# Kernel optimization log

Hardware: AMD Instinct MI355X
Metric: run time of the kernel (lower is better)

Reference implementation:

```python
import jax, jax.numpy as jnp
import numpy as np

N_NODES = 50000
N_EDGES = 800000
HID = 64
N_LAYERS = 3
N_GRAPHS = 64
NEG_SLOPE = 0.01  # nn.LeakyReLU default


def setup_inputs() -> dict:
    key = jax.random.key(0)
    ks = jax.random.split(key, 10)
    return {
        "x": jax.random.normal(ks[0], (N_NODES, HID), dtype=jnp.float32),
        "edge_attr": jax.random.normal(ks[1], (N_EDGES,), dtype=jnp.float32),
        "edge_w": jax.random.normal(ks[2], (N_LAYERS, 1, HID), dtype=jnp.float32) * 0.1,
        "edge_b": jax.random.normal(ks[3], (N_LAYERS, HID), dtype=jnp.float32) * 0.1,
        "node_w": jax.random.normal(ks[4], (N_LAYERS, 2 * HID, HID), dtype=jnp.float32) * 0.05,
        "node_b": jax.random.normal(ks[5], (N_LAYERS, HID), dtype=jnp.float32) * 0.1,
        "fc_w": jax.random.normal(ks[6], (HID, 1), dtype=jnp.float32) * 0.1,
        "fc_b": jax.random.normal(ks[7], (1,), dtype=jnp.float32) * 0.1,
        "edge_index": jax.random.randint(ks[8], (2, N_EDGES), 0, N_NODES, dtype=jnp.int32),
        "batch": jnp.sort(jax.random.randint(ks[9], (N_NODES,), 0, N_GRAPHS, dtype=jnp.int32)),
    }


def reference(x, edge_attr, edge_w, edge_b, node_w, node_b, fc_w, fc_b, edge_index, batch):
    src = edge_index[0]  # x_j gathered from source nodes
    dst = edge_index[1]  # aggregated into target nodes (aggr='add')
    ea = edge_attr.reshape(-1, 1)  # [E, 1]
    for l in range(N_LAYERS):
        edge_emb = ea @ edge_w[l] + edge_b[l]                       # [E, H] edge MLP
        msg = jnp.concatenate([x[src], edge_emb], axis=1)            # [E, 2H] message
        aggr = jax.ops.segment_sum(msg, dst, num_segments=N_NODES)   # [N, 2H] scatter-add
        x = jax.nn.relu(aggr @ node_w[l] + node_b[l])                # update: node MLP + ReLU
        x = jnp.where(x >= 0, x, NEG_SLOPE * x)                      # LeakyReLU (dropout=0)
    # global_mean_pool over batch assignment
    sums = jax.ops.segment_sum(x, batch, num_segments=N_GRAPHS)      # [G, H]
    counts = jax.ops.segment_sum(jnp.ones((x.shape[0], 1), x.dtype), batch, num_segments=N_GRAPHS)
    pooled = sums / jnp.maximum(counts, 1.0)
    return pooled @ fc_w + fc_b  # [G, 1]
```

## Files before the change

kernel.cpp:

```cpp
#include <hip/hip_runtime.h>

#define N_NODES 50000
#define N_EDGES 800000
#define HID 64
#define N_LAYERS 3
#define N_GRAPHS 64
#define MAXDEG 64
#define FIXS 4096.0f
#define CNTSTRIDE 32

typedef unsigned int u32;
typedef unsigned short ushort_t;
typedef short bf16x8 __attribute__((ext_vector_type(8)));
typedef float f32x4 __attribute__((ext_vector_type(4)));

__device__ __forceinline__ ushort_t f2bf(float f) {
    unsigned int u = __builtin_bit_cast(unsigned int, f);
    unsigned int r = u + 0x7fffu + ((u >> 16) & 1u);
    return (ushort_t)(r >> 16);
}
__device__ __forceinline__ float lo16(u32 u) { return __builtin_bit_cast(float, u << 16); }
__device__ __forceinline__ float hi16(u32 u) { return __builtin_bit_cast(float, u & 0xffff0000u); }

__global__ __launch_bounds__(256) void edge_cvt_uv_kernel(
        const int* __restrict__ src, const int* __restrict__ dst,
        const float* __restrict__ ea,
        int* __restrict__ cnt, u32* __restrict__ ell,
        const float* __restrict__ x_in, uint4* __restrict__ xbf0,
        const int* __restrict__ batch, int* __restrict__ gstart,
        const float* __restrict__ edge_w, const float* __restrict__ edge_b,
        const float* __restrict__ node_w, float* __restrict__ uv,
        int edgeBlocks, int cvtBlocks, int gbBlocks) {
    int t = threadIdx.x;
    int b = (int)blockIdx.x;
    if (b < edgeBlocks) {
        int e = b * 256 + t;
        if (e >= N_EDGES) return;
        int d = dst[e];
        float fv = (ea[e] + 8.0f) * FIXS;
        fv = fminf(fmaxf(fv, 0.0f), 65535.0f);
        u32 fx = __float2uint_rn(fv);
        int pos = atomicAdd(&cnt[(size_t)d * CNTSTRIDE], 1);
        if (pos < MAXDEG) ell[((size_t)d << 6) + pos] = (u32)src[e] | (fx << 16);
        return;
    }
    if (b < edgeBlocks + cvtBlocks) {
        int i = (b - edgeBlocks) * 256 + t;
        if (i < N_NODES * HID / 8) {
            const float4* p = (const float4*)(x_in + (size_t)i * 8);
            float4 a = p[0], c = p[1];
            uint4 o;
            o.x = (u32)f2bf(a.x) | ((u32)f2bf(a.y) << 16);
            o.y = (u32)f2bf(a.z) | ((u32)f2bf(a.w) << 16);
            o.z = (u32)f2bf(c.x) | ((u32)f2bf(c.y) << 16);
            o.w = (u32)f2bf(c.z) | ((u32)f2bf(c.w) << 16);
            xbf0[i] = o;
        }
        return;
    }
    if (b < edgeBlocks + cvtBlocks + gbBlocks) {
        int i = (b - edgeBlocks - cvtBlocks) * 256 + t;
        if (i >= N_NODES) return;
        int bi = batch[i];
        if (i == 0) {
            for (int g = 0; g <= bi; g++) gstart[g] = 0;
        } else {
            int bp = batch[i - 1];
            for (int g = bp + 1; g <= bi; g++) gstart[g] = i;
        }
        if (i == N_NODES - 1) {
            for (int g = bi + 1; g <= N_GRAPHS; g++) gstart[g] = N_NODES;
        }
        return;
    }
    if (t >= N_LAYERS * HID) return;
    int l = t >> 6, hp = t & 63;
    const float* w2 = node_w + l * 2 * HID * HID + HID * HID + hp;
    float u = 0.f, v = 0.f;
    for (int h = 0; h < HID; h++) {
        float w = w2[h * HID];
        u += edge_w[l * HID + h] * w;
        v += edge_b[l * HID + h] * w;
    }
    uv[l * 2 * HID + hp]       = u;
    uv[l * 2 * HID + HID + hp] = v;
}

__global__ __launch_bounds__(256) void agg_mfma_kernel(
        const ushort_t* __restrict__ xbf, const u32* __restrict__ ell,
        const int* __restrict__ cnt,
        const float* __restrict__ W1, const float* __restrict__ node_b_l,
        const float* __restrict__ uv_l, float* __restrict__ sattr,
        int layer0, ushort_t* __restrict__ out_bf, float* __restrict__ out_f32) {
    __shared__ float redA[3][64][9];
    __shared__ float redB[3][64][9];
    __shared__ u32   redS[3][64];
    int lane = threadIdx.x & 63;
    int w = threadIdx.x >> 6;
    int nodeBase = blockIdx.x * 16;
    int q = lane >> 4, n15 = lane & 15;

    int m = nodeBase + n15;
    int dg = cnt[(size_t)m * CNTSTRIDE]; if (dg > MAXDEG) dg = MAXDEG;
    int mx = dg;
#pragma unroll
    for (int off = 1; off < 16; off <<= 1) {
        int o = __shfl_xor(mx, off);
        mx = o > mx ? o : mx;
    }

    const uint4* erow4 = (const uint4*)(ell + ((size_t)m << 6));
    const uint4* xrows = (const uint4*)xbf;
    float accA[8] = {0,0,0,0,0,0,0,0};
    float accB[8] = {0,0,0,0,0,0,0,0};
    u32 sfix = 0;
    int base = w * 4;
    uint4 e4 = {0, 0, 0, 0};
    if (base < mx) e4 = erow4[base >> 2];
    for (; base < mx; base += 16) {
        int nbase = base + 16;
        uint4 e4n = {0, 0, 0, 0};
        if (nbase < mx) e4n = erow4[nbase >> 2];
        u32 ee[4] = {e4.x, e4.y, e4.z, e4.w};
        uint4 lo[4], hi[4];
        float f[4];
#pragma unroll
        for (int k = 0; k < 4; k++) {
            bool v = (base + k) < dg;
            u32 e = ee[k];
            sfix += v ? (e >> 16) : 0u;
            int s = v ? (int)(e & 0xffffu) : 0;
            lo[k] = xrows[(size_t)s * 8 + q];
            hi[k] = xrows[(size_t)s * 8 + 4 + q];
            f[k] = v ? 1.0f : 0.0f;
        }
#pragma unroll
        for (int k = 0; k < 4; k++) {
            accA[0] += f[k] * lo16(lo[k].x); accA[1] += f[k] * hi16(lo[k].x);
            accA[2] += f[k] * lo16(lo[k].y); accA[3] += f[k] * hi16(lo[k].y);
            accA[4] += f[k] * lo16(lo[k].z); accA[5] += f[k] * hi16(lo[k].z);
            accA[6] += f[k] * lo16(lo[k].w); accA[7] += f[k] * hi16(lo[k].w);
            accB[0] += f[k] * lo16(hi[k].x); accB[1] += f[k] * hi16(hi[k].x);
            accB[2] += f[k] * lo16(hi[k].y); accB[3] += f[k] * hi16(hi[k].y);
            accB[4] += f[k] * lo16(hi[k].z); accB[5] += f[k] * hi16(hi[k].z);
            accB[6] += f[k] * lo16(hi[k].w); accB[7] += f[k] * hi16(hi[k].w);
        }
        e4 = e4n;
    }

    if (w != 0) {
#pragma unroll
        for (int j = 0; j < 8; j++) { redA[w - 1][lane][j] = accA[j]; redB[w - 1][lane][j] = accB[j]; }
        redS[w - 1][lane] = sfix;
    }
    __syncthreads();
    if (w != 0) return;
#pragma unroll
    for (int p = 0; p < 3; p++) {
#pragma unroll
        for (int j = 0; j < 8; j++) { accA[j] += redA[p][lane][j]; accB[j] += redB[p][lane][j]; }
        sfix += redS[p][lane];
    }

    float satv;
    if (layer0) {
        satv = (float)(int)sfix * (1.0f / FIXS) - 8.0f * (float)dg;
        if (lane < 16) sattr[nodeBase + lane] = satv;
    } else {
        satv = sattr[m];
    }

    bf16x8 af0, af1;
#pragma unroll
    for (int j = 0; j < 8; j++) {
        af0[j] = (short)f2bf(accA[j]);
        af1[j] = (short)f2bf(accB[j]);
    }

    int q8 = q * 8;
    f32x4 c[4];
#pragma unroll
    for (int nt = 0; nt < 4; nt++) {
        bf16x8 b0, b1;
#pragma unroll
        for (int j = 0; j < 8; j++) {
            b0[j] = (short)f2bf(W1[(q8 + j) * HID + nt * 16 + n15]);
            b1[j] = (short)f2bf(W1[(32 + q8 + j) * HID + nt * 16 + n15]);
        }
        f32x4 z = {0.f, 0.f, 0.f, 0.f};
        c[nt] = __builtin_amdgcn_mfma_f32_16x16x32_bf16(af0, b0, z, 0, 0, 0);
        c[nt] = __builtin_amdgcn_mfma_f32_16x16x32_bf16(af1, b1, c[nt], 0, 0, 0);
    }

    float dgown = (float)dg;
    float sat[4], dgf[4];
#pragma unroll
    for (int r = 0; r < 4; r++) {
        int srcLane = q * 4 + r;
        sat[r] = __shfl(satv, srcLane);
        dgf[r] = __shfl(dgown, srcLane);
    }
#pragma unroll
    for (int nt = 0; nt < 4; nt++) {
        int col = nt * 16 + n15;
        float uc = uv_l[col], vc = uv_l[HID + col], bc = node_b_l[col];
#pragma unroll
        for (int r = 0; r < 4; r++) {
            int n = nodeBase + q * 4 + r;
            float val = c[nt][r] + sat[r] * uc + dgf[r] * vc + bc;
            val = val > 0.f ? val : 0.f;
            if (out_bf) out_bf[(size_t)n * HID + col] = f2bf(val);
            else        out_f32[(size_t)n * HID + col] = val;
        }
    }
}

__global__ __launch_bounds__(256) void pool_fc_kernel(
        const float* __restrict__ x, const int* __restrict__ gstart,
        const float* __restrict__ fc_w, const float* __restrict__ fc_b,
        float* __restrict__ out) {
    __shared__ float red[4][HID];
    int g = blockIdx.x;
    int lane = threadIdx.x & 63, w = threadIdx.x >> 6;
    int s = gstart[g], e = gstart[g + 1];
    float acc = 0.f;
    int r = s + w;
    for (; r + 12 < e; r += 16) {
        float a0 = x[(size_t)(r     ) * HID + lane];
        float a1 = x[(size_t)(r +  4) * HID + lane];
        float a2 = x[(size_t)(r +  8) * HID + lane];
        float a3 = x[(size_t)(r + 12) * HID + lane];
        acc += a0 + a1 + a2 + a3;
    }
    for (; r < e; r += 4) acc += x[(size_t)r * HID + lane];
    red[w][lane] = acc;
    __syncthreads();
    if (w != 0) return;
    acc = red[0][lane] + red[1][lane] + red[2][lane] + red[3][lane];
    float dot = acc * fc_w[lane];
    for (int off = 32; off > 0; off >>= 1) dot += __shfl_down(dot, off);
    if (lane == 0) {
        float cntf = (float)(e - s);
        if (cntf < 1.f) cntf = 1.f;
        out[g] = dot / cntf + fc_b[0];
    }
}

extern "C" void kernel_launch(void* const* d_in, const int* in_sizes, int n_in,
                              void* d_out, int out_size, void* d_ws, size_t ws_size,
                              hipStream_t stream) {
    const float* x_in      = (const float*)d_in[0];
    const float* edge_attr = (const float*)d_in[1];
    const float* edge_w    = (const float*)d_in[2];
    const float* edge_b    = (const float*)d_in[3];
    const float* node_w    = (const float*)d_in[4];
    const float* node_b    = (const float*)d_in[5];
    const float* fc_w      = (const float*)d_in[6];
    const float* fc_b      = (const float*)d_in[7];
    const int*   edge_index= (const int*)d_in[8];
    const int*   batch     = (const int*)d_in[9];
    float* out = (float*)d_out;

    ushort_t* xbf0  = (ushort_t*)d_ws;
    ushort_t* xbf1  = xbf0 + (size_t)N_NODES * HID;
    float*    xA    = (float*)(xbf1 + (size_t)N_NODES * HID);
    u32*      ell   = (u32*)(xA + (size_t)N_NODES * HID);
    int*      cnt   = (int*)(ell + (size_t)N_NODES * MAXDEG);
    int*      gstart= cnt + (size_t)N_NODES * CNTSTRIDE;
    float*    sattr = (float*)(gstart + N_GRAPHS + 1);
    float*    uv    = sattr + N_NODES;

    const int* src = edge_index;
    const int* dst = edge_index + N_EDGES;

    hipMemsetAsync(cnt, 0, (size_t)N_NODES * CNTSTRIDE * sizeof(int), stream);

    const int EB  = (N_EDGES + 255) / 256;
    const int CVT = (N_NODES * HID / 8 + 255) / 256;
    const int GB  = (N_NODES + 255) / 256;
    edge_cvt_uv_kernel<<<EB + CVT + GB + 1, 256, 0, stream>>>(
        src, dst, edge_attr, cnt, ell, x_in, (uint4*)xbf0, batch, gstart,
        edge_w, edge_b, node_w, uv, EB, CVT, GB);

    const int AGG_BLOCKS = N_NODES / 16;
    agg_mfma_kernel<<<AGG_BLOCKS, 256, 0, stream>>>(
        xbf0, ell, cnt, node_w, node_b, uv, sattr, 1, xbf1, nullptr);
    agg_mfma_kernel<<<AGG_BLOCKS, 256, 0, stream>>>(
        xbf1, ell, cnt, node_w + (size_t)2 * HID * HID, node_b + HID, uv + 2 * HID,
        sattr, 0, xbf0, nullptr);
    agg_mfma_kernel<<<AGG_BLOCKS, 256, 0, stream>>>(
        xbf0, ell, cnt, node_w + (size_t)4 * HID * HID, node_b + 2 * HID, uv + 4 * HID,
        sattr, 0, nullptr, xA);

    pool_fc_kernel<<<N_GRAPHS, 256, 0, stream>>>(xA, gstart, fc_w, fc_b, out);
}
```

Baseline: 219.6 us.

## Split node features into lo/hi planes and aggregate in two passes

```diff
diff --git a/kernel.cpp b/kernel.cpp
--- a/kernel.cpp
+++ b/kernel.cpp
@@ -26,7 +26,8 @@
         const int* __restrict__ src, const int* __restrict__ dst,
         const float* __restrict__ ea,
         int* __restrict__ cnt, u32* __restrict__ ell,
-        const float* __restrict__ x_in, uint4* __restrict__ xbf0,
+        const float* __restrict__ x_in,
+        uint4* __restrict__ lo_plane, uint4* __restrict__ hi_plane,
         const int* __restrict__ batch, int* __restrict__ gstart,
         const float* __restrict__ edge_w, const float* __restrict__ edge_b,
         const float* __restrict__ node_w, float* __restrict__ uv,
@@ -54,7 +55,9 @@
             o.y = (u32)f2bf(a.z) | ((u32)f2bf(a.w) << 16);
             o.z = (u32)f2bf(c.x) | ((u32)f2bf(c.y) << 16);
             o.w = (u32)f2bf(c.z) | ((u32)f2bf(c.w) << 16);
-            xbf0[i] = o;
+            int row = i >> 3, g = i & 7;
+            if (g < 4) lo_plane[(size_t)row * 4 + g]       = o;
+            else       hi_plane[(size_t)row * 4 + (g - 4)] = o;
         }
         return;
     }
@@ -86,20 +89,81 @@
     uv[l * 2 * HID + HID + hp] = v;
 }
 
-__global__ __launch_bounds__(256) void agg_mfma_kernel(
-        const ushort_t* __restrict__ xbf, const u32* __restrict__ ell,
-        const int* __restrict__ cnt,
+__global__ __launch_bounds__(256) void agg_lo_kernel(
+        const uint4* __restrict__ xplane, const u32* __restrict__ ell,
+        const int* __restrict__ cnt, uint4* __restrict__ aggLO) {
+    __shared__ float redA[3][64][9];
+    int lane = threadIdx.x & 63;
+    int w = threadIdx.x >> 6;
+    int nodeBase = blockIdx.x * 16;
+    int q = lane >> 4, n15 = lane & 15;
+    int m = nodeBase + n15;
+    int dg = cnt[(size_t)m * CNTSTRIDE]; if (dg > MAXDEG) dg = MAXDEG;
+    int mx = dg;
+#pragma unroll
+    for (int off = 1; off < 16; off <<= 1) {
+        int o = __shfl_xor(mx, off);
+        mx = o > mx ? o : mx;
+    }
+    const uint4* erow4 = (const uint4*)(ell + ((size_t)m << 6));
+    float accA[8] = {0,0,0,0,0,0,0,0};
+    int base = w * 4;
+    uint4 e4 = {0, 0, 0, 0};
+    if (base < mx) e4 = erow4[base >> 2];
+    for (; base < mx; base += 16) {
+        int nbase = base + 16;
+        uint4 e4n = {0, 0, 0, 0};
+        if (nbase < mx) e4n = erow4[nbase >> 2];
+        u32 ee[4] = {e4.x, e4.y, e4.z, e4.w};
+        uint4 lo[4];
+        float f[4];
+#pragma unroll
+        for (int k = 0; k < 4; k++) {
+            bool v = (base + k) < dg;
+            int s = v ? (int)(ee[k] & 0xffffu) : 0;
+            lo[k] = xplane[(size_t)s * 4 + q];
+            f[k] = v ? 1.0f : 0.0f;
+        }
+#pragma unroll
+        for (int k = 0; k < 4; k++) {
+            accA[0] += f[k] * lo16(lo[k].x); accA[1] += f[k] * hi16(lo[k].x);
+            accA[2] += f[k] * lo16(lo[k].y); accA[3] += f[k] * hi16(lo[k].y);
+            accA[4] += f[k] * lo16(lo[k].z); accA[5] += f[k] * hi16(lo[k].z);
+            accA[6] += f[k] * lo16(lo[k].w); accA[7] += f[k] * hi16(lo[k].w);
+        }
+        e4 = e4n;
+    }
+    if (w != 0) {
+#pragma unroll
+        for (int j = 0; j < 8; j++) redA[w - 1][lane][j] = accA[j];
+    }
+    __syncthreads();
+    if (w != 0) return;
+#pragma unroll
+    for (int p = 0; p < 3; p++)
+#pragma unroll
+        for (int j = 0; j < 8; j++) accA[j] += redA[p][lane][j];
+    uint4 o;
+    o.x = (u32)f2bf(accA[0]) | ((u32)f2bf(accA[1]) << 16);
+    o.y = (u32)f2bf(accA[2]) | ((u32)f2bf(accA[3]) << 16);
+    o.z = (u32)f2bf(accA[4]) | ((u32)f2bf(accA[5]) << 16);
+    o.w = (u32)f2bf(accA[6]) | ((u32)f2bf(accA[7]) << 16);
+    aggLO[(size_t)m * 4 + q] = o;
+}
+
+__global__ __launch_bounds__(256) void agg_hi_mfma_kernel(
+        const uint4* __restrict__ xplane, const uint4* __restrict__ aggLO,
+        const u32* __restrict__ ell, const int* __restrict__ cnt,
         const float* __restrict__ W1, const float* __restrict__ node_b_l,
         const float* __restrict__ uv_l, float* __restrict__ sattr,
-        int layer0, ushort_t* __restrict__ out_bf, float* __restrict__ out_f32) {
-    __shared__ float redA[3][64][9];
+        int layer0, ushort_t* __restrict__ out_lo, ushort_t* __restrict__ out_hi,
+        float* __restrict__ out_f32) {
     __shared__ float redB[3][64][9];
     __shared__ u32   redS[3][64];
     int lane = threadIdx.x & 63;
     int w = threadIdx.x >> 6;
     int nodeBase = blockIdx.x * 16;
     int q = lane >> 4, n15 = lane & 15;
-
     int m = nodeBase + n15;
     int dg = cnt[(size_t)m * CNTSTRIDE]; if (dg > MAXDEG) dg = MAXDEG;
     int mx = dg;
@@ -108,10 +172,7 @@
         int o = __shfl_xor(mx, off);
         mx = o > mx ? o : mx;
     }
-
     const uint4* erow4 = (const uint4*)(ell + ((size_t)m << 6));
-    const uint4* xrows = (const uint4*)xbf;
-    float accA[8] = {0,0,0,0,0,0,0,0};
     float accB[8] = {0,0,0,0,0,0,0,0};
     u32 sfix = 0;
     int base = w * 4;
@@ -122,7 +183,7 @@
         uint4 e4n = {0, 0, 0, 0};
         if (nbase < mx) e4n = erow4[nbase >> 2];
         u32 ee[4] = {e4.x, e4.y, e4.z, e4.w};
-        uint4 lo[4], hi[4];
+        uint4 hi[4];
         float f[4];
 #pragma unroll
         for (int k = 0; k < 4; k++) {
@@ -130,16 +191,11 @@
             u32 e = ee[k];
             sfix += v ? (e >> 16) : 0u;
             int s = v ? (int)(e & 0xffffu) : 0;
-            lo[k] = xrows[(size_t)s * 8 + q];
-            hi[k] = xrows[(size_t)s * 8 + 4 + q];
+            hi[k] = xplane[(size_t)s * 4 + q];
             f[k] = v ? 1.0f : 0.0f;
         }
 #pragma unroll
         for (int k = 0; k < 4; k++) {
-            accA[0] += f[k] * lo16(lo[k].x); accA[1] += f[k] * hi16(lo[k].x);
-            accA[2] += f[k] * lo16(lo[k].y); accA[3] += f[k] * hi16(lo[k].y);
-            accA[4] += f[k] * lo16(lo[k].z); accA[5] += f[k] * hi16(lo[k].z);
-            accA[6] += f[k] * lo16(lo[k].w); accA[7] += f[k] * hi16(lo[k].w);
             accB[0] += f[k] * lo16(hi[k].x); accB[1] += f[k] * hi16(hi[k].x);
             accB[2] += f[k] * lo16(hi[k].y); accB[3] += f[k] * hi16(hi[k].y);
             accB[4] += f[k] * lo16(hi[k].z); accB[5] += f[k] * hi16(hi[k].z);
@@ -147,10 +203,9 @@
         }
         e4 = e4n;
     }
-
     if (w != 0) {
 #pragma unroll
-        for (int j = 0; j < 8; j++) { redA[w - 1][lane][j] = accA[j]; redB[w - 1][lane][j] = accB[j]; }
+        for (int j = 0; j < 8; j++) redB[w - 1][lane][j] = accB[j];
         redS[w - 1][lane] = sfix;
     }
     __syncthreads();
@@ -158,7 +213,7 @@
 #pragma unroll
     for (int p = 0; p < 3; p++) {
 #pragma unroll
-        for (int j = 0; j < 8; j++) { accA[j] += redA[p][lane][j]; accB[j] += redB[p][lane][j]; }
+        for (int j = 0; j < 8; j++) accB[j] += redB[p][lane][j];
         sfix += redS[p][lane];
     }
 
@@ -170,12 +225,10 @@
         satv = sattr[m];
     }
 
-    bf16x8 af0, af1;
-#pragma unroll
-    for (int j = 0; j < 8; j++) {
-        af0[j] = (short)f2bf(accA[j]);
-        af1[j] = (short)f2bf(accB[j]);
-    }
+    bf16x8 af0 = *(const bf16x8*)&aggLO[(size_t)m * 4 + q];
+    bf16x8 af1;
+#pragma unroll
+    for (int j = 0; j < 8; j++) af1[j] = (short)f2bf(accB[j]);
 
     int q8 = q * 8;
     f32x4 c[4];
@@ -209,8 +262,12 @@
             int n = nodeBase + q * 4 + r;
             float val = c[nt][r] + sat[r] * uc + dgf[r] * vc + bc;
             val = val > 0.f ? val : 0.f;
-            if (out_bf) out_bf[(size_t)n * HID + col] = f2bf(val);
-            else        out_f32[(size_t)n * HID + col] = val;
+            if (out_f32) {
+                out_f32[(size_t)n * HID + col] = val;
+            } else {
+                ushort_t* pl = (nt < 2) ? out_lo : out_hi;
+                pl[(size_t)n * 32 + (col & 31)] = f2bf(val);
+            }
         }
     }
 }
@@ -261,14 +318,17 @@
     const int*   batch     = (const int*)d_in[9];
     float* out = (float*)d_out;
 
-    ushort_t* xbf0  = (ushort_t*)d_ws;
-    ushort_t* xbf1  = xbf0 + (size_t)N_NODES * HID;
-    float*    xA    = (float*)(xbf1 + (size_t)N_NODES * HID);
-    u32*      ell   = (u32*)(xA + (size_t)N_NODES * HID);
-    int*      cnt   = (int*)(ell + (size_t)N_NODES * MAXDEG);
-    int*      gstart= cnt + (size_t)N_NODES * CNTSTRIDE;
-    float*    sattr = (float*)(gstart + N_GRAPHS + 1);
-    float*    uv    = sattr + N_NODES;
+    ushort_t* loA  = (ushort_t*)d_ws;
+    ushort_t* hiA  = loA + (size_t)N_NODES * 32;
+    ushort_t* loB  = hiA + (size_t)N_NODES * 32;
+    ushort_t* hiB  = loB + (size_t)N_NODES * 32;
+    ushort_t* agl  = hiB + (size_t)N_NODES * 32;
+    float*    xA   = (float*)(agl + (size_t)N_NODES * 32);
+    u32*      ell  = (u32*)(xA + (size_t)N_NODES * HID);
+    int*      cnt  = (int*)(ell + (size_t)N_NODES * MAXDEG);
+    int*      gstart = cnt + (size_t)N_NODES * CNTSTRIDE;
+    float*    sattr  = (float*)(gstart + N_GRAPHS + 1);
+    float*    uv     = sattr + N_NODES;
 
     const int* src = edge_index;
     const int* dst = edge_index + N_EDGES;
@@ -279,18 +339,22 @@
     const int CVT = (N_NODES * HID / 8 + 255) / 256;
     const int GB  = (N_NODES + 255) / 256;
     edge_cvt_uv_kernel<<<EB + CVT + GB + 1, 256, 0, stream>>>(
-        src, dst, edge_attr, cnt, ell, x_in, (uint4*)xbf0, batch, gstart,
+        src, dst, edge_attr, cnt, ell, x_in, (uint4*)loA, (uint4*)hiA, batch, gstart,
         edge_w, edge_b, node_w, uv, EB, CVT, GB);
 
     const int AGG_BLOCKS = N_NODES / 16;
-    agg_mfma_kernel<<<AGG_BLOCKS, 256, 0, stream>>>(
-        xbf0, ell, cnt, node_w, node_b, uv, sattr, 1, xbf1, nullptr);
-    agg_mfma_kernel<<<AGG_BLOCKS, 256, 0, stream>>>(
-        xbf1, ell, cnt, node_w + (size_t)2 * HID * HID, node_b + HID, uv + 2 * HID,
-        sattr, 0, xbf0, nullptr);
-    agg_mfma_kernel<<<AGG_BLOCKS, 256, 0, stream>>>(
-        xbf0, ell, cnt, node_w + (size_t)4 * HID * HID, node_b + 2 * HID, uv + 4 * HID,
-        sattr, 0, nullptr, xA);
+    agg_lo_kernel<<<AGG_BLOCKS, 256, 0, stream>>>((uint4*)loA, ell, cnt, (uint4*)agl);
+    agg_hi_mfma_kernel<<<AGG_BLOCKS, 256, 0, stream>>>(
+        (uint4*)hiA, (uint4*)agl, ell, cnt, node_w, node_b, uv, sattr, 1,
+        loB, hiB, nullptr);
+    agg_lo_kernel<<<AGG_BLOCKS, 256, 0, stream>>>((uint4*)loB, ell, cnt, (uint4*)agl);
+    agg_hi_mfma_kernel<<<AGG_BLOCKS, 256, 0, stream>>>(
+        (uint4*)hiB, (uint4*)agl, ell, cnt, node_w + (size_t)2 * HID * HID,
+        node_b + HID, uv + 2 * HID, sattr, 0, loA, hiA, nullptr);
+    agg_lo_kernel<<<AGG_BLOCKS, 256, 0, stream>>>((uint4*)loA, ell, cnt, (uint4*)agl);
+    agg_hi_mfma_kernel<<<AGG_BLOCKS, 256, 0, stream>>>(
+        (uint4*)hiA, (uint4*)agl, ell, cnt, node_w + (size_t)4 * HID * HID,
+        node_b + 2 * HID, uv + 4 * HID, sattr, 0, nullptr, nullptr, xA);
 
     pool_fc_kernel<<<N_GRAPHS, 256, 0, stream>>>(xA, gstart, fc_w, fc_b, out);
 }
```

New measurement: 231.3 us. 5.3% more time.

## Remap gather lanes to 8-node-per-wave layout and split pooling across blocks

Applied to the files above, without the earlier changes.

```diff
diff --git a/kernel.cpp b/kernel.cpp
--- a/kernel.cpp
+++ b/kernel.cpp
@@ -30,6 +30,7 @@
         const int* __restrict__ batch, int* __restrict__ gstart,
         const float* __restrict__ edge_w, const float* __restrict__ edge_b,
         const float* __restrict__ node_w, float* __restrict__ uv,
+        const float* __restrict__ fc_b, float* __restrict__ out,
         int edgeBlocks, int cvtBlocks, int gbBlocks) {
     int t = threadIdx.x;
     int b = (int)blockIdx.x;
@@ -73,7 +74,10 @@
         }
         return;
     }
-    if (t >= N_LAYERS * HID) return;
+    if (t >= 192) {
+        if (t < 192 + N_GRAPHS) out[t - 192] = fc_b[0];
+        return;
+    }
     int l = t >> 6, hp = t & 63;
     const float* w2 = node_w + l * 2 * HID * HID + HID * HID + hp;
     float u = 0.f, v = 0.f;
@@ -92,82 +96,81 @@
         const float* __restrict__ W1, const float* __restrict__ node_b_l,
         const float* __restrict__ uv_l, float* __restrict__ sattr,
         int layer0, ushort_t* __restrict__ out_bf, float* __restrict__ out_f32) {
-    __shared__ float redA[3][64][9];
-    __shared__ float redB[3][64][9];
-    __shared__ u32   redS[3][64];
+    __shared__ float red[4][64][9];
+    __shared__ u32   redS[4][8];
     int lane = threadIdx.x & 63;
     int w = threadIdx.x >> 6;
     int nodeBase = blockIdx.x * 16;
-    int q = lane >> 4, n15 = lane & 15;
-
-    int m = nodeBase + n15;
+    int oct = lane & 7, n8 = lane >> 3;
+    int pairSel = w >> 1;
+    int kslice = w & 1;
+
+    int m = nodeBase + pairSel * 8 + n8;
     int dg = cnt[(size_t)m * CNTSTRIDE]; if (dg > MAXDEG) dg = MAXDEG;
     int mx = dg;
 #pragma unroll
-    for (int off = 1; off < 16; off <<= 1) {
+    for (int off = 8; off < 64; off <<= 1) {
         int o = __shfl_xor(mx, off);
         mx = o > mx ? o : mx;
     }
 
     const uint4* erow4 = (const uint4*)(ell + ((size_t)m << 6));
     const uint4* xrows = (const uint4*)xbf;
-    float accA[8] = {0,0,0,0,0,0,0,0};
-    float accB[8] = {0,0,0,0,0,0,0,0};
+    float accC[8] = {0,0,0,0,0,0,0,0};
     u32 sfix = 0;
-    int base = w * 4;
+    int base = kslice * 4;
     uint4 e4 = {0, 0, 0, 0};
     if (base < mx) e4 = erow4[base >> 2];
-    for (; base < mx; base += 16) {
-        int nbase = base + 16;
+    for (; base < mx; base += 8) {
+        int nbase = base + 8;
         uint4 e4n = {0, 0, 0, 0};
         if (nbase < mx) e4n = erow4[nbase >> 2];
         u32 ee[4] = {e4.x, e4.y, e4.z, e4.w};
-        uint4 lo[4], hi[4];
+        uint4 rw[4];
         float f[4];
 #pragma unroll
         for (int k = 0; k < 4; k++) {
             bool v = (base + k) < dg;
-            u32 e = ee[k];
-            sfix += v ? (e >> 16) : 0u;
-            int s = v ? (int)(e & 0xffffu) : 0;
-            lo[k] = xrows[(size_t)s * 8 + q];
-            hi[k] = xrows[(size_t)s * 8 + 4 + q];
+            sfix += (v && oct == 0) ? (ee[k] >> 16) : 0u;
+            int s = v ? (int)(ee[k] & 0xffffu) : 0;
+            rw[k] = xrows[(size_t)s * 8 + oct];
             f[k] = v ? 1.0f : 0.0f;
         }
 #pragma unroll
         for (int k = 0; k < 4; k++) {
-            accA[0] += f[k] * lo16(lo[k].x); accA[1] += f[k] * hi16(lo[k].x);
-            accA[2] += f[k] * lo16(lo[k].y); accA[3] += f[k] * hi16(lo[k].y);
-            accA[4] += f[k] * lo16(lo[k].z); accA[5] += f[k] * hi16(lo[k].z);
-            accA[6] += f[k] * lo16(lo[k].w); accA[7] += f[k] * hi16(lo[k].w);
-            accB[0] += f[k] * lo16(hi[k].x); accB[1] += f[k] * hi16(hi[k].x);
-            accB[2] += f[k] * lo16(hi[k].y); accB[3] += f[k] * hi16(hi[k].y);
-            accB[4] += f[k] * lo16(hi[k].z); accB[5] += f[k] * hi16(hi[k].z);
-            accB[6] += f[k] * lo16(hi[k].w); accB[7] += f[k] * hi16(hi[k].w);
+            accC[0] += f[k] * lo16(rw[k].x); accC[1] += f[k] * hi16(rw[k].x);
+            accC[2] += f[k] * lo16(rw[k].y); accC[3] += f[k] * hi16(rw[k].y);
+            accC[4] += f[k] * lo16(rw[k].z); accC[5] += f[k] * hi16(rw[k].z);
+            accC[6] += f[k] * lo16(rw[k].w); accC[7] += f[k] * hi16(rw[k].w);
         }
         e4 = e4n;
     }
 
-    if (w != 0) {
-#pragma unroll
-        for (int j = 0; j < 8; j++) { redA[w - 1][lane][j] = accA[j]; redB[w - 1][lane][j] = accB[j]; }
-        redS[w - 1][lane] = sfix;
-    }
+#pragma unroll
+    for (int j = 0; j < 8; j++) red[w][lane][j] = accC[j];
+    if (oct == 0) redS[w][n8] = sfix;
     __syncthreads();
     if (w != 0) return;
-#pragma unroll
-    for (int p = 0; p < 3; p++) {
-#pragma unroll
-        for (int j = 0; j < 8; j++) { accA[j] += redA[p][lane][j]; accB[j] += redB[p][lane][j]; }
-        sfix += redS[p][lane];
-    }
+
+    int q = lane >> 4, n15 = lane & 15;
+    int w0 = (n15 >> 3) * 2;
+    int h8 = (n15 & 7) * 8;
+    float accA[8], accB[8];
+#pragma unroll
+    for (int j = 0; j < 8; j++) {
+        accA[j] = red[w0][h8 + q][j]     + red[w0 + 1][h8 + q][j];
+        accB[j] = red[w0][h8 + 4 + q][j] + red[w0 + 1][h8 + 4 + q][j];
+    }
+    u32 sfix2 = redS[w0][n15 & 7] + redS[w0 + 1][n15 & 7];
+    int m2 = nodeBase + n15;
+    int dg2 = cnt[(size_t)m2 * CNTSTRIDE]; if (dg2 > MAXDEG) dg2 = MAXDEG;
 
     float satv;
     if (layer0) {
-        satv = (float)(int)sfix * (1.0f / FIXS) - 8.0f * (float)dg;
-        if (lane < 16) sattr[nodeBase + lane] = satv;
+        satv = (float)(int)sfix2 * (1.0f / FIXS) - 8.0f * (float)dg2;
+        if (lane < 16) sattr[m2] = satv;
     } else {
-        satv = sattr[m];
+        satv = sattr[m2];
     }
 
     bf16x8 af0, af1;
@@ -192,7 +195,7 @@
         c[nt] = __builtin_amdgcn_mfma_f32_16x16x32_bf16(af1, b1, c[nt], 0, 0, 0);
     }
 
-    float dgown = (float)dg;
+    float dgown = (float)dg2;
     float sat[4], dgf[4];
 #pragma unroll
     for (int r = 0; r < 4; r++) {
@@ -217,22 +220,21 @@
 
 __global__ __launch_bounds__(256) void pool_fc_kernel(
         const float* __restrict__ x, const int* __restrict__ gstart,
-        const float* __restrict__ fc_w, const float* __restrict__ fc_b,
-        float* __restrict__ out) {
+        const float* __restrict__ fc_w, float* __restrict__ out) {
     __shared__ float red[4][HID];
-    int g = blockIdx.x;
+    int g = blockIdx.x >> 3, s8 = blockIdx.x & 7;
     int lane = threadIdx.x & 63, w = threadIdx.x >> 6;
     int s = gstart[g], e = gstart[g + 1];
     float acc = 0.f;
-    int r = s + w;
-    for (; r + 12 < e; r += 16) {
+    int r = s + s8 * 4 + w;
+    for (; r + 96 < e; r += 128) {
         float a0 = x[(size_t)(r     ) * HID + lane];
-        float a1 = x[(size_t)(r +  4) * HID + lane];
-        float a2 = x[(size_t)(r +  8) * HID + lane];
-        float a3 = x[(size_t)(r + 12) * HID + lane];
+        float a1 = x[(size_t)(r + 32) * HID + lane];
+        float a2 = x[(size_t)(r + 64) * HID + lane];
+        float a3 = x[(size_t)(r + 96) * HID + lane];
         acc += a0 + a1 + a2 + a3;
     }
-    for (; r < e; r += 4) acc += x[(size_t)r * HID + lane];
+    for (; r < e; r += 32) acc += x[(size_t)r * HID + lane];
     red[w][lane] = acc;
     __syncthreads();
     if (w != 0) return;
@@ -242,7 +244,7 @@
     if (lane == 0) {
         float cntf = (float)(e - s);
         if (cntf < 1.f) cntf = 1.f;
-        out[g] = dot / cntf + fc_b[0];
+        atomicAdd(&out[g], dot / cntf);
     }
 }
 
@@ -280,7 +282,7 @@
     const int GB  = (N_NODES + 255) / 256;
     edge_cvt_uv_kernel<<<EB + CVT + GB + 1, 256, 0, stream>>>(
         src, dst, edge_attr, cnt, ell, x_in, (uint4*)xbf0, batch, gstart,
-        edge_w, edge_b, node_w, uv, EB, CVT, GB);
+        edge_w, edge_b, node_w, uv, fc_b, out, EB, CVT, GB);
 
     const int AGG_BLOCKS = N_NODES / 16;
     agg_mfma_kernel<<<AGG_BLOCKS, 256, 0, stream>>>(
@@ -292,5 +294,5 @@
         xbf0, ell, cnt, node_w + (size_t)4 * HID * HID, node_b + 2 * HID, uv + 4 * HID,
         sattr, 0, nullptr, xA);
 
-    pool_fc_kernel<<<N_GRAPHS, 256, 0, stream>>>(xA, gstart, fc_w, fc_b, out);
-}
+    pool_fc_kernel<<<N_GRAPHS * 8, 256, 0, stream>>>(xA, gstart, fc_w, out);
+}
```

Result: faster. 189.3 us (-13.8%).
